# Performance work log

Hardware: AMD Instinct MI355X
Metric: run time of the kernel (lower is better)

## Reference

```python
import jax, jax.numpy as jnp
import numpy as np
from jax import lax

KERNEL = 3
K = 3


def setup_inputs() -> dict:
    key = jax.random.key(0)
    xcorr = jax.random.normal(key, (16, 1, 256, 8192), dtype=jnp.float32)
    return {"xcorr": xcorr}


def reference(xcorr):
    # xcorr: [B, C, H, W] (W = lag axis)
    W = xcorr.shape[-1]
    nlag = W // 2
    # max_pool2d with kernel (1,KERNEL), stride 1, padding (0, KERNEL//2).
    # torch pads with -inf for max pooling.
    neg_inf = jnp.asarray(-jnp.inf, dtype=xcorr.dtype)
    pad = KERNEL // 2
    smax = lax.reduce_window(
        xcorr,
        neg_inf,
        lax.max,
        window_dimensions=(1, 1, 1, KERNEL),
        window_strides=(1, 1, 1, 1),
        padding=[(0, 0), (0, 0), (0, 0), (pad, pad)],
    )
    keep = (smax == xcorr).astype(xcorr.dtype)  # local-max NMS mask
    scores = xcorr * keep
    topk_scores, topk_inds = lax.top_k(scores, K)  # sorted descending, [B,C,H,K]
    top = topk_inds[..., 0]  # best peak index [B,C,H]
    nearby = jnp.clip(
        jnp.stack([top - 1, top, top + 1], axis=-1), 0, W - 1
    )  # [B,C,H,3]
    neighbor_score = jnp.take_along_axis(xcorr, nearby, axis=-1)
    topk_index = topk_inds - nlag
    return neighbor_score, topk_scores, topk_index
```

## Files before the change

kernel.cpp:

```cpp
#include <hip/hip_runtime.h>
#include <climits>
#include <cmath>


#define PW    8192
#define PNLAG (PW / 2)
#define BLOCK 256
#define NW    4
#define J     8
#define CHUNK 2048
#define CPR   4

__device__ __forceinline__ bool better(float av, int ai, float bv, int bi) {
  return (av > bv) || ((av == bv) && (ai < bi));
}

__device__ __forceinline__ void insert3_full(float v, int i,
                                             float &v0, int &i0,
                                             float &v1, int &i1,
                                             float &v2, int &i2) {
  if (better(v, i, v2, i2)) {
    if (better(v, i, v1, i1)) {
      if (better(v, i, v0, i0)) {
        v2 = v1; i2 = i1; v1 = v0; i1 = i0; v0 = v; i0 = i;
      } else {
        v2 = v1; i2 = i1; v1 = v; i1 = i;
      }
    } else {
      v2 = v; i2 = i;
    }
  }
}

__device__ __forceinline__ void insert3_fast(float c, int ci,
                                             float &v0, int &i0,
                                             float &v1, int &i1,
                                             float &v2, int &i2) {
  const bool b2 = c > v2;
  const bool b1 = c > v1;
  const bool b0 = c > v0;
  v2 = b1 ? v1 : (b2 ? c : v2);  i2 = b1 ? i1 : (b2 ? ci : i2);
  v1 = b0 ? v0 : (b1 ? c : v1);  i1 = b0 ? i0 : (b1 ? ci : i1);
  v0 = b0 ? c  : v0;             i0 = b0 ? ci : i0;
}

__global__ __launch_bounds__(BLOCK, 4)
void peaks_pass1(const float* __restrict__ x, float* __restrict__ ws) {
  const int t     = threadIdx.x;
  const int lane  = t & 63;
  const int wave  = t >> 6;
  const int chunk = blockIdx.x * NW + wave;
  const int row   = chunk >> 2;
  const int c     = chunk & 3;
  const float* __restrict__ xr = x + (size_t)row * PW;
  const int base  = c * CHUNK;

  const float edgeL = (base > 0)          ? xr[base - 1]     : -INFINITY;
  const float edgeR = (base + CHUNK < PW) ? xr[base + CHUNK] : -INFINITY;

  float4 q[J];
#pragma unroll
  for (int j = 0; j < J; ++j)
    q[j] = *(const float4*)(xr + base + (j * 64 + lane) * 4);

  float v0 = -INFINITY, v1 = -INFINITY, v2 = -INFINITY;
  int   i0 = INT_MAX,   i1 = INT_MAX,   i2 = INT_MAX;

#pragma unroll
  for (int j = 0; j < J; ++j) {
    const float4 v = q[j];

    float left = __shfl_up(v.w, 1);
    const float lf = (j == 0) ? edgeL : __shfl(q[j - 1].w, 63);
    if (lane == 0) left = lf;
    float right = __shfl_down(v.x, 1);
    const float rf = (j == J - 1) ? edgeR : __shfl(q[j + 1].x, 0);
    if (lane == 63) right = rf;

    const int p = base + (j * 64 + lane) * 4;

    const float p01 = fmaxf(v.x, v.y);
    const float p12 = fmaxf(v.y, v.z);
    const float p23 = fmaxf(v.z, v.w);
    const float m0 = fmaxf(left, p01);
    const float m1 = fmaxf(p01, v.z);
    const float m2 = fmaxf(p12, v.w);
    const float m3 = fmaxf(p23, right);

    const float s0 = (v.x == m0) ? v.x : 0.0f;
    const float s1 = (v.y == m1) ? v.y : 0.0f;
    const float s2 = (v.z == m2) ? v.z : 0.0f;
    const float s3 = (v.w == m3) ? v.w : 0.0f;

    const bool  a01 = s0 >= s1;
    const float hiA = a01 ? s0 : s1;   const int hiAi = a01 ? p     : p + 1;
    const float loA = a01 ? s1 : s0;   const int loAi = a01 ? p + 1 : p;
    const bool  a23 = s2 >= s3;
    const float hiB = a23 ? s2 : s3;   const int hiBi = a23 ? p + 2 : p + 3;
    const float loB = a23 ? s3 : s2;   const int loBi = a23 ? p + 3 : p + 2;

    const bool  ab  = hiA >= hiB;
    const float c1  = ab ? hiA : hiB;  const int c1i = ab ? hiAi : hiBi;
    const bool  sb  = ab ? (loA >= hiB) : (hiA >= loB);
    const float c2  = ab ? (sb ? loA : hiB) : (sb ? hiA : loB);
    const int   c2i = ab ? (sb ? loAi : hiBi) : (sb ? hiAi : loBi);

    insert3_fast(c1, c1i, v0, i0, v1, i1, v2, i2);
    insert3_fast(c2, c2i, v0, i0, v1, i1, v2, i2);
  }

#pragma unroll
  for (int off = 32; off > 0; off >>= 1) {
    float ov0 = __shfl_down(v0, off);
    int   oi0 = __shfl_down(i0, off);
    float ov1 = __shfl_down(v1, off);
    int   oi1 = __shfl_down(i1, off);
    float ov2 = __shfl_down(v2, off);
    int   oi2 = __shfl_down(i2, off);
    if (lane + off < 64) {
      insert3_full(ov0, oi0, v0, i0, v1, i1, v2, i2);
      insert3_full(ov1, oi1, v0, i0, v1, i1, v2, i2);
      insert3_full(ov2, oi2, v0, i0, v1, i1, v2, i2);
    }
  }

  if (lane == 0) {
    float* o = ws + (size_t)chunk * 8;
    float4 vv; vv.x = v0; vv.y = v1; vv.z = v2; vv.w = 0.0f;
    *(float4*)o = vv;
    int4 ii; ii.x = i0; ii.y = i1; ii.z = i2; ii.w = 0;
    *(int4*)(o + 4) = ii;
  }
}

__global__ __launch_bounds__(BLOCK)
void peaks_pass2(const float* __restrict__ x, const float* __restrict__ ws,
                 float* __restrict__ out, int rows) {
  const int row = blockIdx.x * BLOCK + threadIdx.x;
  if (row >= rows) return;

  float v0 = -INFINITY, v1 = -INFINITY, v2 = -INFINITY;
  int   i0 = INT_MAX,   i1 = INT_MAX,   i2 = INT_MAX;

#pragma unroll
  for (int c = 0; c < CPR; ++c) {
    const float* o = ws + ((size_t)row * CPR + c) * 8;
    const float4 vv = *(const float4*)o;
    const int4   ii = *(const int4*)(o + 4);
    insert3_full(vv.x, ii.x, v0, i0, v1, i1, v2, i2);
    insert3_full(vv.y, ii.y, v0, i0, v1, i1, v2, i2);
    insert3_full(vv.z, ii.z, v0, i0, v1, i1, v2, i2);
  }

  const float* __restrict__ xr = x + (size_t)row * PW;
  float* __restrict__ nb = out;
  float* __restrict__ ts = out + (size_t)rows * 3;
  float* __restrict__ ti = out + (size_t)rows * 6;

  const int top = i0;
#pragma unroll
  for (int k = 0; k < 3; ++k) {
    int idx = top - 1 + k;
    idx = idx < 0 ? 0 : (idx > PW - 1 ? PW - 1 : idx);
    nb[row * 3 + k] = xr[idx];
  }
  ts[row * 3 + 0] = v0;
  ts[row * 3 + 1] = v1;
  ts[row * 3 + 2] = v2;
  ti[row * 3 + 0] = (float)(i0 - PNLAG);
  ti[row * 3 + 1] = (float)(i1 - PNLAG);
  ti[row * 3 + 2] = (float)(i2 - PNLAG);
}

extern "C" void kernel_launch(void* const* d_in, const int* in_sizes, int n_in,
                              void* d_out, int out_size, void* d_ws, size_t ws_size,
                              hipStream_t stream) {
  const float* x = (const float*)d_in[0];
  float* out = (float*)d_out;
  float* ws  = (float*)d_ws;
  const int rows = in_sizes[0] / PW;

  peaks_pass1<<<rows * CPR / NW, BLOCK, 0, stream>>>(x, ws);
  peaks_pass2<<<(rows + BLOCK - 1) / BLOCK, BLOCK, 0, stream>>>(x, ws, out, rows);
}
```

Baseline: 243.5 us.

## Use persistent grid-stride waves with a rolling one-ahead load pipeline in pass1

Pass1 becomes a persistent kernel with a fixed grid of 2048 blocks, where each wave grid-strides over chunks. Inside each chunk, the eight float4 loads that were previously all issued up front are replaced by a loop that prefetches only the next segment, with a carry value for the left neighbor. This lowers register pressure and removes the per-chunk block launches. The trade-off is less memory-level parallelism per wave, since only one load is in flight ahead. The chunk count is hardcoded as 4096 rows times 4 chunks, which ties the kernel to the test shape.

```diff
diff --git a/kernel.cpp b/kernel.cpp
--- a/kernel.cpp
+++ b/kernel.cpp
@@ -7,9 +7,12 @@
 #define PNLAG (PW / 2)
 #define BLOCK 256
 #define NW    4
-#define J     8
 #define CHUNK 2048
 #define CPR   4
+#define SEGS  8
+#define GRID1 2048
+#define NCHUNK (4096 * CPR)
+#define TOTW  (GRID1 * NW)
 
 __device__ __forceinline__ bool better(float av, int ai, float bv, int bi) {
   return (av > bv) || ((av == bv) && (ai < bi));
@@ -44,92 +47,98 @@
   v0 = b0 ? c  : v0;             i0 = b0 ? ci : i0;
 }
 
-__global__ __launch_bounds__(BLOCK, 4)
+__global__ __launch_bounds__(BLOCK)
 void peaks_pass1(const float* __restrict__ x, float* __restrict__ ws) {
-  const int t     = threadIdx.x;
-  const int lane  = t & 63;
-  const int wave  = t >> 6;
-  const int chunk = blockIdx.x * NW + wave;
-  const int row   = chunk >> 2;
-  const int c     = chunk & 3;
-  const float* __restrict__ xr = x + (size_t)row * PW;
-  const int base  = c * CHUNK;
+  const int t    = threadIdx.x;
+  const int lane = t & 63;
+  const int wave = t >> 6;
+  const int wgid = blockIdx.x * NW + wave;
 
-  const float edgeL = (base > 0)          ? xr[base - 1]     : -INFINITY;
-  const float edgeR = (base + CHUNK < PW) ? xr[base + CHUNK] : -INFINITY;
+  for (int chunk = wgid; chunk < NCHUNK; chunk += TOTW) {
+    const int row  = chunk >> 2;
+    const int c    = chunk & 3;
+    const int base = c * CHUNK;
+    const float* __restrict__ xr = x + (size_t)row * PW;
 
-  float4 q[J];
-#pragma unroll
-  for (int j = 0; j < J; ++j)
-    q[j] = *(const float4*)(xr + base + (j * 64 + lane) * 4);
+    const float edgeL = (base > 0)          ? xr[base - 1]     : -INFINITY;
+    const float edgeR = (base + CHUNK < PW) ? xr[base + CHUNK] : -INFINITY;
 
-  float v0 = -INFINITY, v1 = -INFINITY, v2 = -INFINITY;
-  int   i0 = INT_MAX,   i1 = INT_MAX,   i2 = INT_MAX;
+    float v0 = -INFINITY, v1 = -INFINITY, v2 = -INFINITY;
+    int   i0 = INT_MAX,   i1 = INT_MAX,   i2 = INT_MAX;
+
+    float4 cur = *(const float4*)(xr + base + lane * 4);
+    float carry = edgeL;
+
+#pragma unroll 1
+    for (int s = 0; s < SEGS; ++s) {
+      const bool last = (s == SEGS - 1);
+      float4 nxt = cur;
+      if (!last)
+        nxt = *(const float4*)(xr + base + (s + 1) * 256 + lane * 4);
+
+      float left = __shfl_up(cur.w, 1);
+      if (lane == 0) left = carry;
+      const float nf = last ? edgeR : __shfl(nxt.x, 0);
+      float right = __shfl_down(cur.x, 1);
+      if (lane == 63) right = nf;
+      carry = __shfl(cur.w, 63);
+
+      const int p = base + s * 256 + lane * 4;
+
+      const float p01 = fmaxf(cur.x, cur.y);
+      const float p12 = fmaxf(cur.y, cur.z);
+      const float p23 = fmaxf(cur.z, cur.w);
+      const float m0 = fmaxf(left, p01);
+      const float m1 = fmaxf(p01, cur.z);
+      const float m2 = fmaxf(p12, cur.w);
+      const float m3 = fmaxf(p23, right);
+
+      const float s0 = (cur.x == m0) ? cur.x : 0.0f;
+      const float s1 = (cur.y == m1) ? cur.y : 0.0f;
+      const float s2 = (cur.z == m2) ? cur.z : 0.0f;
+      const float s3 = (cur.w == m3) ? cur.w : 0.0f;
+
+      const bool  a01 = s0 >= s1;
+      const float hiA = a01 ? s0 : s1;   const int hiAi = a01 ? p     : p + 1;
+      const float loA = a01 ? s1 : s0;   const int loAi = a01 ? p + 1 : p;
+      const bool  a23 = s2 >= s3;
+      const float hiB = a23 ? s2 : s3;   const int hiBi = a23 ? p + 2 : p + 3;
+      const float loB = a23 ? s3 : s2;   const int loBi = a23 ? p + 3 : p + 2;
+
+      const bool  ab  = hiA >= hiB;
+      const float c1  = ab ? hiA : hiB;  const int c1i = ab ? hiAi : hiBi;
+      const bool  sb  = ab ? (loA >= hiB) : (hiA >= loB);
+      const float c2  = ab ? (sb ? loA : hiB) : (sb ? hiA : loB);
+      const int   c2i = ab ? (sb ? loAi : hiBi) : (sb ? hiAi : loBi);
+
+      insert3_fast(c1, c1i, v0, i0, v1, i1, v2, i2);
+      insert3_fast(c2, c2i, v0, i0, v1, i1, v2, i2);
+
+      cur = nxt;
+    }
 
 #pragma unroll
-  for (int j = 0; j < J; ++j) {
-    const float4 v = q[j];
+    for (int off = 32; off > 0; off >>= 1) {
+      float ov0 = __shfl_down(v0, off);
+      int   oi0 = __shfl_down(i0, off);
+      float ov1 = __shfl_down(v1, off);
+      int   oi1 = __shfl_down(i1, off);
+      float ov2 = __shfl_down(v2, off);
+      int   oi2 = __shfl_down(i2, off);
+      if (lane + off < 64) {
+        insert3_full(ov0, oi0, v0, i0, v1, i1, v2, i2);
+        insert3_full(ov1, oi1, v0, i0, v1, i1, v2, i2);
+        insert3_full(ov2, oi2, v0, i0, v1, i1, v2, i2);
+      }
+    }
 
-    float left = __shfl_up(v.w, 1);
-    const float lf = (j == 0) ? edgeL : __shfl(q[j - 1].w, 63);
-    if (lane == 0) left = lf;
-    float right = __shfl_down(v.x, 1);
-    const float rf = (j == J - 1) ? edgeR : __shfl(q[j + 1].x, 0);
-    if (lane == 63) right = rf;
-
-    const int p = base + (j * 64 + lane) * 4;
-
-    const float p01 = fmaxf(v.x, v.y);
-    const float p12 = fmaxf(v.y, v.z);
-    const float p23 = fmaxf(v.z, v.w);
-    const float m0 = fmaxf(left, p01);
-    const float m1 = fmaxf(p01, v.z);
-    const float m2 = fmaxf(p12, v.w);
-    const float m3 = fmaxf(p23, right);
-
-    const float s0 = (v.x == m0) ? v.x : 0.0f;
-    const float s1 = (v.y == m1) ? v.y : 0.0f;
-    const float s2 = (v.z == m2) ? v.z : 0.0f;
-    const float s3 = (v.w == m3) ? v.w : 0.0f;
-
-    const bool  a01 = s0 >= s1;
-    const float hiA = a01 ? s0 : s1;   const int hiAi = a01 ? p     : p + 1;
-    const float loA = a01 ? s1 : s0;   const int loAi = a01 ? p + 1 : p;
-    const bool  a23 = s2 >= s3;
-    const float hiB = a23 ? s2 : s3;   const int hiBi = a23 ? p + 2 : p + 3;
-    const float loB = a23 ? s3 : s2;   const int loBi = a23 ? p + 3 : p + 2;
-
-    const bool  ab  = hiA >= hiB;
-    const float c1  = ab ? hiA : hiB;  const int c1i = ab ? hiAi : hiBi;
-    const bool  sb  = ab ? (loA >= hiB) : (hiA >= loB);
-    const float c2  = ab ? (sb ? loA : hiB) : (sb ? hiA : loB);
-    const int   c2i = ab ? (sb ? loAi : hiBi) : (sb ? hiAi : loBi);
-
-    insert3_fast(c1, c1i, v0, i0, v1, i1, v2, i2);
-    insert3_fast(c2, c2i, v0, i0, v1, i1, v2, i2);
-  }
-
-#pragma unroll
-  for (int off = 32; off > 0; off >>= 1) {
-    float ov0 = __shfl_down(v0, off);
-    int   oi0 = __shfl_down(i0, off);
-    float ov1 = __shfl_down(v1, off);
-    int   oi1 = __shfl_down(i1, off);
-    float ov2 = __shfl_down(v2, off);
-    int   oi2 = __shfl_down(i2, off);
-    if (lane + off < 64) {
-      insert3_full(ov0, oi0, v0, i0, v1, i1, v2, i2);
-      insert3_full(ov1, oi1, v0, i0, v1, i1, v2, i2);
-      insert3_full(ov2, oi2, v0, i0, v1, i1, v2, i2);
+    if (lane == 0) {
+      float* o = ws + (size_t)chunk * 8;
+      float4 vv; vv.x = v0; vv.y = v1; vv.z = v2; vv.w = 0.0f;
+      *(float4*)o = vv;
+      int4 ii; ii.x = i0; ii.y = i1; ii.z = i2; ii.w = 0;
+      *(int4*)(o + 4) = ii;
     }
-  }
-
-  if (lane == 0) {
-    float* o = ws + (size_t)chunk * 8;
-    float4 vv; vv.x = v0; vv.y = v1; vv.z = v2; vv.w = 0.0f;
-    *(float4*)o = vv;
-    int4 ii; ii.x = i0; ii.y = i1; ii.z = i2; ii.w = 0;
-    *(int4*)(o + 4) = ii;
   }
 }
 
@@ -180,6 +189,6 @@
   float* ws  = (float*)d_ws;
   const int rows = in_sizes[0] / PW;
 
-  peaks_pass1<<<rows * CPR / NW, BLOCK, 0, stream>>>(x, ws);
+  peaks_pass1<<<GRID1, BLOCK, 0, stream>>>(x, ws);
   peaks_pass2<<<(rows + BLOCK - 1) / BLOCK, BLOCK, 0, stream>>>(x, ws, out, rows);
 }
```

Measured after the change: 251.7 us. 1.03x slower.
